# Optimization experiments

Hardware: AMD Instinct MI355X
Metric: run time of the kernel (lower is better)

The kernel has to match this reference:

```python
import jax, jax.numpy as jnp
import numpy as np

NUM_TASKS = 150
ACT_DIM = 4
ENC_DIM = 256
EMB_DIM = 32
HEAD_HID = 128
B, H, W = 256, 128, 128


def _conv(x, w, b):
    # x: NCHW, w: OIHW, stride 2, padding 1 (torch Conv2d semantics)
    y = jax.lax.conv_general_dilated(x, w, window_strides=(2, 2),
                                     padding=((1, 1), (1, 1)),
                                     dimension_numbers=('NCHW', 'OIHW', 'NCHW'))
    return y + b[None, :, None, None]


def setup_inputs() -> dict:
    key = jax.random.key(0)
    ks = iter(jax.random.split(key, 32))
    s = 0.05
    d = {
        'images': jax.random.normal(next(ks), (B, 3, H, W), jnp.float32),
        'proprioception': jax.random.normal(next(ks), (B, 7), jnp.float32),
        'task_ids': jax.random.randint(next(ks), (B,), 0, NUM_TASKS, jnp.int32),
        # vision encoder convs (OIHW)
        'c1_w': jax.random.normal(next(ks), (64, 3, 3, 3), jnp.float32) * s,
        'c1_b': jnp.zeros((64,), jnp.float32),
        'c2_w': jax.random.normal(next(ks), (128, 64, 3, 3), jnp.float32) * s,
        'c2_b': jnp.zeros((128,), jnp.float32),
        'c3_w': jax.random.normal(next(ks), (256, 128, 3, 3), jnp.float32) * s,
        'c3_b': jnp.zeros((256,), jnp.float32),
        # proprioception encoder (weights stored as [in, out])
        'p1_w': jax.random.normal(next(ks), (7, 64), jnp.float32) * s,
        'p1_b': jnp.zeros((64,), jnp.float32),
        'p2_w': jax.random.normal(next(ks), (64, 64), jnp.float32) * s,
        'p2_b': jnp.zeros((64,), jnp.float32),
        # shared-encoder fusion MLP (320 -> 256 -> 256)
        'f1_w': jax.random.normal(next(ks), (256 + 64, ENC_DIM), jnp.float32) * s,
        'f1_b': jnp.zeros((ENC_DIM,), jnp.float32),
        'f2_w': jax.random.normal(next(ks), (ENC_DIM, ENC_DIM), jnp.float32) * s,
        'f2_b': jnp.zeros((ENC_DIM,), jnp.float32),
        # task embedding table
        'task_emb': jax.random.normal(next(ks), (NUM_TASKS, EMB_DIM), jnp.float32) * s,
        # policy-level fusion (288 -> 256), dropout is identity at inference
        'g_w': jax.random.normal(next(ks), (ENC_DIM + EMB_DIM, ENC_DIM), jnp.float32) * s,
        'g_b': jnp.zeros((ENC_DIM,), jnp.float32),
        # stacked task-specific heads [num_tasks, in, out]
        'h1_w': jax.random.normal(next(ks), (NUM_TASKS, ENC_DIM, HEAD_HID), jnp.float32) * s,
        'h1_b': jnp.zeros((NUM_TASKS, HEAD_HID), jnp.float32),
        'h2_w': jax.random.normal(next(ks), (NUM_TASKS, HEAD_HID, HEAD_HID), jnp.float32) * s,
        'h2_b': jnp.zeros((NUM_TASKS, HEAD_HID), jnp.float32),
        'h3_w': jax.random.normal(next(ks), (NUM_TASKS, HEAD_HID, ACT_DIM), jnp.float32) * s,
        'h3_b': jnp.zeros((NUM_TASKS, ACT_DIM), jnp.float32),
    }
    return d


def reference(images, proprioception, task_ids,
              c1_w, c1_b, c2_w, c2_b, c3_w, c3_b,
              p1_w, p1_b, p2_w, p2_b,
              f1_w, f1_b, f2_w, f2_b,
              task_emb, g_w, g_b,
              h1_w, h1_b, h2_w, h2_b, h3_w, h3_b):
    relu = jax.nn.relu
    # vision encoder: 3 strided convs + global avg pool (AdaptiveAvgPool2d(1,1))
    v = relu(_conv(images, c1_w, c1_b))
    v = relu(_conv(v, c2_w, c2_b))
    v = relu(_conv(v, c3_w, c3_b))
    v = jnp.mean(v, axis=(2, 3))                      # [B, 256]
    # proprioception encoder (no final ReLU)
    p = relu(proprioception @ p1_w + p1_b) @ p2_w + p2_b  # [B, 64]
    # shared fusion
    f = relu(jnp.concatenate([v, p], axis=1) @ f1_w + f1_b)
    f = relu(f @ f2_w + f2_b)                         # [B, 256]
    # task embedding + policy fusion (dropout = identity in eval)
    e = task_emb[task_ids]                            # [B, 32]
    z = relu(jnp.concatenate([f, e], axis=1) @ g_w + g_b)  # [B, 256]
    # routed task heads: gather per-sample expert params, batched matmuls
    a = relu(jnp.einsum('bd,bdh->bh', z, h1_w[task_ids]) + h1_b[task_ids])
    a = relu(jnp.einsum('bd,bdh->bh', a, h2_w[task_ids]) + h2_b[task_ids])
    a = jnp.einsum('bd,bdh->bh', a, h3_w[task_ids]) + h3_b[task_ids]  # [B, 4]
    return a
```

## Files before the change

### kernel.cpp

```cpp
#include <hip/hip_runtime.h>
#include <hip/hip_bf16.h>

#define DIV_UP(a,b) (((a)+(b)-1)/(b))

typedef __attribute__((ext_vector_type(8))) short short8;
typedef __attribute__((ext_vector_type(4))) float f32x4;

__device__ __forceinline__ ushort bf16_bits(float x) {
    return __builtin_bit_cast(ushort, __float2bfloat16(x));
}

__device__ __forceinline__ void gload_lds16(const ushort* g, ushort* l) {
    __builtin_amdgcn_global_load_lds(
        (const __attribute__((address_space(1))) void*)g,
        (__attribute__((address_space(3))) void*)l, 16, 0, 0);
}

__global__ __launch_bounds__(256) void prep_kernel(
    uint4* __restrict__ act1, uint4* __restrict__ act2,
    float4* __restrict__ vbuf, int CHI,
    const float* __restrict__ c1_w, __hip_bfloat16* __restrict__ w1b,
    const float* __restrict__ c2_w, __hip_bfloat16* __restrict__ w2t,
    const float* __restrict__ c3_w, __hip_bfloat16* __restrict__ w3t) {
    const int tid = threadIdx.x;
    int bx = blockIdx.x;

    if (bx < CHI) {
        const int b = bx;
        const uint4 z = {0u, 0u, 0u, 0u};
        uint4* a1 = act1 + (size_t)b * 33800;
        for (int i = tid; i < 520; i += 256) a1[i] = z;
        for (int i = tid; i < 512; i += 256) {
            int r = (i >> 3) + 1;
            a1[r * 520 + (i & 7)] = z;
        }
        uint4* a2 = act2 + (size_t)b * 17424;
        for (int i = tid; i < 528; i += 256) a2[i] = z;
        for (int i = tid; i < 512; i += 256) {
            int r = (i >> 4) + 1;
            a2[r * 528 + (i & 15)] = z;
        }
        int idx = b * 256 + tid;
        float4 zf = {0.f, 0.f, 0.f, 0.f};
        if (idx < 16384) vbuf[idx] = zf;
        return;
    }
    bx -= CHI;

    if (bx < 8) {
        int t = bx * 256 + tid;
        int k  = t & 31;
        int oc = t >> 5;
        w1b[t] = (k < 27) ? __float2bfloat16(c1_w[oc * 27 + k])
                          : __float2bfloat16(0.f);
        return;
    }
    bx -= 8;

    const float* src;
    __hip_bfloat16* dst;
    int O, C, t;
    if (bx < 288) {
        src = c2_w; dst = w2t; O = 128; C = 64;
        t = bx * 256 + tid;
    } else {
        src = c3_w; dst = w3t; O = 256; C = 128;
        t = (bx - 288) * 256 + tid;
    }
    int e   = t & 7;
    int r   = t >> 3;
    int n   = r % O;
    int q   = r / O;
    int SEG = C >> 3;
    int sg  = q % SEG;
    int tap = q / SEG;
    dst[t] = __float2bfloat16(src[(n * C + sg * 8 + e) * 9 + tap]);
}

__global__ __launch_bounds__(256) void conv1_mfma_kernel(
    const float* __restrict__ in,
    const __hip_bfloat16* __restrict__ wB,
    const float* __restrict__ bias,
    __hip_bfloat16* __restrict__ out) {
    const int tid  = threadIdx.x;
    const int lane = tid & 63;
    const int wv   = tid >> 6;
    const int l15  = lane & 15;
    const int quad = lane >> 4;
    const int tile = blockIdx.x;
    const int b    = blockIdx.y;
    const int oh0  = tile << 2;

    __shared__ __align__(16) char smem[30208];
    float*  sx = (float*)smem;
    ushort* Al = (ushort*)(smem + 13824);

    const float* ip  = in + (size_t)b * 3 * 128 * 128;
    const int    ih0 = 2 * oh0 - 1;

#pragma unroll
    for (int it = 0; it < 4; ++it) {
        int e = (it << 8) + tid;
        if (e < 864) {
            int q = e >> 5, k = e & 31;
            int c = q / 9, r = q - c * 9;
            int row = ih0 + r;
            if (row < 0) row = 0;
            gload_lds16((const ushort*)(ip + c * 16384 + row * 128 + k * 4),
                        (ushort*)smem + (size_t)e * 8);
        }
    }
    __syncthreads();

    const int px = tid, ohl = px >> 6, ow = px & 63;
    union { uint4 u4[4]; ushort us[32]; } rowv;
#pragma unroll
    for (int c = 0; c < 3; ++c)
#pragma unroll
        for (int kh = 0; kh < 3; ++kh) {
            const bool rok = (ih0 + 2 * ohl + kh) >= 0;
            const float* srow = sx + (c * 9 + 2 * ohl + kh) * 128;
#pragma unroll
            for (int kw = 0; kw < 3; ++kw) {
                int iw = 2 * ow + kw - 1;
                bool ok = rok && (iw >= 0);
                float x = srow[iw < 0 ? 0 : iw];
                rowv.us[c * 9 + kh * 3 + kw] = bf16_bits(ok ? x : 0.f);
            }
        }
#pragma unroll
    for (int k = 27; k < 32; ++k) rowv.us[k] = 0;
#pragma unroll
    for (int q = 0; q < 4; ++q)
        *(uint4*)(Al + px * 32 + (((q ^ (px >> 1)) & 3) << 3)) = rowv.u4[q];

    short8 af[4], bf[4];
#pragma unroll
    for (int i = 0; i < 4; ++i)
        af[i] = __builtin_bit_cast(short8,
            *(const uint4*)(wB + ((i * 16 + l15) * 32 + quad * 8)));

    __syncthreads();

#pragma unroll
    for (int j = 0; j < 4; ++j) {
        int p = wv * 64 + j * 16 + l15;
        bf[j] = __builtin_bit_cast(short8,
            *(const uint4*)(Al + p * 32 + (((quad ^ (p >> 1)) & 3) << 3)));
    }
    f32x4 acc[4][4];
#pragma unroll
    for (int i = 0; i < 4; ++i)
#pragma unroll
        for (int j = 0; j < 4; ++j)
            acc[i][j] = __builtin_amdgcn_mfma_f32_16x16x32_bf16(
                af[i], bf[j], (f32x4){0.f, 0.f, 0.f, 0.f}, 0, 0, 0);

    float4 bv[4];
#pragma unroll
    for (int i = 0; i < 4; ++i)
        bv[i] = *(const float4*)(bias + i * 16 + quad * 4);

    __hip_bfloat16* ob = out + (((size_t)b * 65 + oh0 + 1) * 65 + 1) * 64;
#pragma unroll
    for (int j = 0; j < 4; ++j) {
        const int oww = j * 16 + l15;
        __hip_bfloat16* op = ob + ((size_t)(wv * 65) + oww) * 64 + quad * 4;
#pragma unroll
        for (int i = 0; i < 4; ++i) {
            union { uint2 u2; ushort us[4]; } pk;
#pragma unroll
            for (int r = 0; r < 4; ++r)
                pk.us[r] = bf16_bits(
                    fmaxf(acc[i][j][r] + ((const float*)&bv[i])[r], 0.f));
            *(uint2*)(op + i * 16) = pk.u2;
        }
    }
}

__global__ __launch_bounds__(256, 3) void conv2_gemm_kernel(
    const __hip_bfloat16* __restrict__ act,
    const __hip_bfloat16* __restrict__ wtB,
    const float* __restrict__ bias,
    __hip_bfloat16* __restrict__ out) {
    const int tid  = threadIdx.x;
    const int lane = tid & 63;
    const int w    = tid >> 6;
    const int l15  = lane & 15;
    const int quad = lane >> 4;
    const int per  = gridDim.x >> 3;
    const int Mt   = (blockIdx.x & 7) * per + (blockIdx.x >> 3);
    const int bimg = Mt >> 4;
    const int oh0  = (Mt & 15) << 1;

    __shared__ __align__(16) char smem[41600];
    ushort* As = (ushort*)smem;
    ushort* Cs = (ushort*)smem;

    f32x4 acc[2][4];
#pragma unroll
    for (int i = 0; i < 2; ++i)
#pragma unroll
        for (int j = 0; j < 4; ++j) acc[i][j] = (f32x4){0.f, 0.f, 0.f, 0.f};

    const int pxw = (w >> 1) << 5;
    const int wn  = (w & 1) << 6;
    const size_t abase = ((size_t)(bimg * 65 + 2 * oh0)) * 65 * 64;
    const ushort* ap = (const ushort*)act;

#pragma unroll
    for (int it = 0; it < 11; ++it) {
        int c = (it << 8) + tid;
        if (c < 2600) {
            int p = c >> 3, t = c & 7;
            int q = t ^ ((p >> 1) & 7);
            gload_lds16(ap + abase + (size_t)p * 64 + q * 8,
                        As + (size_t)c * 8);
        }
    }
    __syncthreads();

    for (int h = 0; h < 2; ++h) {
        const int q = h * 4 + quad;
#pragma unroll
        for (int tap = 0; tap < 9; ++tap) {
            const int kh = tap / 3, kw = tap - kh * 3;
            short8 af[2], bf[4];
#pragma unroll
            for (int i = 0; i < 2; ++i) {
                int ml = pxw + i * 16 + l15;
                int p  = ((ml >> 5) * 2 + kh) * 65 + ((ml & 31) * 2 + kw);
                af[i] = __builtin_bit_cast(short8,
                    *(const uint4*)(As + p * 64 +
                                    ((q ^ ((p >> 1) & 7)) << 3)));
            }
#pragma unroll
            for (int j = 0; j < 4; ++j)
                bf[j] = __builtin_bit_cast(short8,
                    *(const uint4*)(wtB +
                        ((size_t)((tap * 8 + h * 4 + quad) * 128) +
                         wn + j * 16 + l15) * 8));
#pragma unroll
            for (int i = 0; i < 2; ++i)
#pragma unroll
                for (int j = 0; j < 4; ++j)
                    acc[i][j] = __builtin_amdgcn_mfma_f32_16x16x32_bf16(
                        af[i], bf[j], acc[i][j], 0, 0, 0);
        }
    }

    __syncthreads();
#pragma unroll
    for (int j = 0; j < 4; ++j) {
        int n = wn + j * 16 + l15;
        float bv = bias[n];
#pragma unroll
        for (int i = 0; i < 2; ++i)
#pragma unroll
            for (int r = 0; r < 4; ++r) {
                int ml = pxw + i * 16 + quad * 4 + r;
                Cs[ml * 132 + n] = bf16_bits(fmaxf(acc[i][j][r] + bv, 0.f));
            }
    }
    __syncthreads();
#pragma unroll
    for (int q2 = 0; q2 < 8; ++q2) {
        int c   = tid + 256 * q2;
        int row = c >> 5;
        int off = c & 31;
        uint2 val = *(const uint2*)(Cs + row * 132 + off * 4);
        int m  = (Mt << 6) + row;
        int b  = m >> 10;
        int rr = m & 1023;
        int oh = rr >> 5;
        int ow = rr & 31;
        size_t pix = ((size_t)(b * 33 + oh + 1) * 33 + (ow + 1));
        *(uint2*)(out + pix * 128 + off * 4) = val;
    }
}

__global__ __launch_bounds__(256, 2) void conv3_gemm_pool_kernel(
    const __hip_bfloat16* __restrict__ act,
    const __hip_bfloat16* __restrict__ wtB,
    const float* __restrict__ bias,
    float* __restrict__ v ) {
    const int tid  = threadIdx.x;
    const int lane = tid & 63;
    const int w    = tid >> 6;
    const int l15  = lane & 15;
    const int quad = lane >> 4;
    const int per  = gridDim.x >> 3;
    const int Mt   = (blockIdx.x & 7) * per + (blockIdx.x >> 3);
    const int bimg = Mt >> 2;
    const int oh0  = (Mt & 3) << 2;

    __shared__ __align__(16) char smem[77824];
    ushort* As   = (ushort*)smem;
    float*  sred = (float*)smem;

    f32x4 acc[4][4];
#pragma unroll
    for (int i = 0; i < 4; ++i)
#pragma unroll
        for (int j = 0; j < 4; ++j) acc[i][j] = (f32x4){0.f, 0.f, 0.f, 0.f};

    const int wn = w << 6;
    const size_t abase = ((size_t)(bimg * 33 + 2 * oh0)) * 33 * 128;
    const ushort* ap = (const ushort*)act;

#pragma unroll
    for (int it = 0; it < 19; ++it) {
        int c  = (it << 8) + tid;
        int p  = c >> 4;
        int t  = c & 15;
        int h  = t >> 3;
        int ss = (t & 7) ^ ((p >> 1) & 7);
        gload_lds16(ap + abase + (size_t)p * 128 + h * 64 + ss * 8,
                    As + (size_t)c * 8);
    }
    __syncthreads();

    for (int h = 0; h < 2; ++h) {
#pragma unroll 1
        for (int tap = 0; tap < 9; ++tap) {
            const int kh = tap / 3, kw = tap - kh * 3;
#pragma unroll
            for (int ks = 0; ks < 2; ++ks) {
                short8 af[4], bf[4];
                const int sl = ks * 4 + quad;
#pragma unroll
                for (int i = 0; i < 4; ++i) {
                    int p = (i * 2 + kh) * 33 + l15 * 2 + kw;
                    af[i] = __builtin_bit_cast(short8,
                        *(const uint4*)(As + p * 128 + h * 64 +
                                        (((sl ^ (p >> 1)) & 7) << 3)));
                }
#pragma unroll
                for (int j = 0; j < 4; ++j)
                    bf[j] = __builtin_bit_cast(short8,
                        *(const uint4*)(wtB +
                            ((size_t)((tap * 16 + h * 8 + sl) * 256) +
                             wn + j * 16 + l15) * 8));
#pragma unroll
                for (int i = 0; i < 4; ++i)
#pragma unroll
                    for (int j = 0; j < 4; ++j)
                        acc[i][j] = __builtin_amdgcn_mfma_f32_16x16x32_bf16(
                            af[i], bf[j], acc[i][j], 0, 0, 0);
            }
        }
    }

    float s4[4];
#pragma unroll
    for (int j = 0; j < 4; ++j) {
        float bv = bias[wn + j * 16 + l15];
        float s = 0.f;
#pragma unroll
        for (int i = 0; i < 4; ++i)
#pragma unroll
            for (int r = 0; r < 4; ++r)
                s += fmaxf(acc[i][j][r] + bv, 0.f);
        s += __shfl_xor(s, 16, 64);
        s += __shfl_xor(s, 32, 64);
        s4[j] = s;
    }
    __syncthreads();
    if (quad == 0) {
#pragma unroll
        for (int j = 0; j < 4; ++j) sred[wn + j * 16 + l15] = s4[j];
    }
    __syncthreads();
    atomicAdd(v + (size_t)bimg * 256 + tid, sred[tid] * (1.f / 256.f));
}

template<int N, int K, int S, bool RELU>
__device__ __forceinline__ void gemv_stage(const float* __restrict__ w,
                                           const float* __restrict__ bias,
                                           const float* in, float* outv,
                                           float4* red4, int tid) {
    constexpr int G = N / 4;
    constexpr int CHK = K / S;
    static_assert(G * S == 256 && CHK * S == K, "stage shape");
    const int g = tid % G, s = tid / G;
    const float4* wp = (const float4*)w;
    float4 a; a.x = a.y = a.z = a.w = 0.f;
    const int k0 = s * CHK;
#pragma unroll 8
    for (int i = 0; i < CHK; ++i) {
        float x = in[k0 + i];
        float4 wv = wp[(size_t)(k0 + i) * G + g];
        a.x = fmaf(x, wv.x, a.x);
        a.y = fmaf(x, wv.y, a.y);
        a.z = fmaf(x, wv.z, a.z);
        a.w = fmaf(x, wv.w, a.w);
    }
    red4[tid] = a;
    __syncthreads();
    if (tid < N) {
        int gg = tid >> 2, e = tid & 3;
        float vv = bias[tid];
#pragma unroll
        for (int ss = 0; ss < S; ++ss) {
            const float* rp = (const float*)(red4 + ss * G + gg);
            vv += rp[e];
        }
        if (RELU) vv = fmaxf(vv, 0.f);
        outv[tid] = vv;
    }
    __syncthreads();
}

__global__ __launch_bounds__(256) void tail_kernel(
    const float* __restrict__ prop, const int* __restrict__ task_ids,
    const float* __restrict__ p1_w, const float* __restrict__ p1_b,
    const float* __restrict__ p2_w, const float* __restrict__ p2_b,
    const float* __restrict__ v,
    const float* __restrict__ f1_w, const float* __restrict__ f1_b,
    const float* __restrict__ f2_w, const float* __restrict__ f2_b,
    const float* __restrict__ task_emb,
    const float* __restrict__ g_w, const float* __restrict__ g_b,
    const float* __restrict__ h1_w, const float* __restrict__ h1_b,
    const float* __restrict__ h2_w, const float* __restrict__ h2_b,
    const float* __restrict__ h3_w, const float* __restrict__ h3_b,
    float* __restrict__ out) {
    const int b   = blockIdx.x;
    const int tid = threadIdx.x;
    const int t   = task_ids[b];
    __shared__ float sa[320];
    __shared__ float sb[288];
    __shared__ float sph[64];
    __shared__ float4 red4[256];

    sa[tid] = (tid < 256) ? v[(size_t)b * 256 + tid] : 0.f;
    if (tid < 64) {
        float h = p1_b[tid];
#pragma unroll
        for (int k = 0; k < 7; ++k) h = fmaf(prop[b * 7 + k], p1_w[k * 64 + tid], h);
        sph[tid] = fmaxf(h, 0.f);
    }
    __syncthreads();
    gemv_stage<64, 64, 16, false>(p2_w, p2_b, sph, sa + 256, red4, tid);
    gemv_stage<256, 320, 4, true>(f1_w, f1_b, sa, sb, red4, tid);
    gemv_stage<256, 256, 4, true>(f2_w, f2_b, sb, sa, red4, tid);
    if (tid < 32) sa[256 + tid] = task_emb[t * 32 + tid];
    __syncthreads();
    gemv_stage<256, 288, 4, true>(g_w, g_b, sa, sb, red4, tid);
    gemv_stage<128, 256, 8, true>(h1_w + (size_t)t * 32768, h1_b + t * 128,
                                  sb, sa, red4, tid);
    gemv_stage<128, 128, 8, true>(h2_w + (size_t)t * 16384, h2_b + t * 128,
                                  sa, sb, red4, tid);
    if (tid < 128) {
        float4 wv = ((const float4*)(h3_w + (size_t)t * 512))[tid];
        float x = sb[tid];
        float r0 = x * wv.x, r1 = x * wv.y, r2 = x * wv.z, r3 = x * wv.w;
#pragma unroll
        for (int off = 1; off < 64; off <<= 1) {
            r0 += __shfl_xor(r0, off, 64);
            r1 += __shfl_xor(r1, off, 64);
            r2 += __shfl_xor(r2, off, 64);
            r3 += __shfl_xor(r3, off, 64);
        }
        if ((tid & 63) == 0) {
            float4 rv; rv.x = r0; rv.y = r1; rv.z = r2; rv.w = r3;
            red4[tid >> 6] = rv;
        }
    }
    __syncthreads();
    if (tid < 4) {
        const float* ra = (const float*)(red4 + 0);
        const float* rb = (const float*)(red4 + 1);
        out[b * 4 + tid] = ra[tid] + rb[tid] + h3_b[t * 4 + tid];
    }
}

extern "C" void kernel_launch(void* const* d_in, const int* in_sizes, int n_in,
                              void* d_out, int out_size, void* d_ws, size_t ws_size,
                              hipStream_t stream) {
    (void)in_sizes; (void)n_in; (void)out_size;
    const float* images   = (const float*)d_in[0];
    const float* prop     = (const float*)d_in[1];
    const int*   task_ids = (const int*)d_in[2];
    const float* c1_w = (const float*)d_in[3];
    const float* c1_b = (const float*)d_in[4];
    const float* c2_w = (const float*)d_in[5];
    const float* c2_b = (const float*)d_in[6];
    const float* c3_w = (const float*)d_in[7];
    const float* c3_b = (const float*)d_in[8];
    const float* p1_w = (const float*)d_in[9];
    const float* p1_b = (const float*)d_in[10];
    const float* p2_w = (const float*)d_in[11];
    const float* p2_b = (const float*)d_in[12];
    const float* f1_w = (const float*)d_in[13];
    const float* f1_b = (const float*)d_in[14];
    const float* f2_w = (const float*)d_in[15];
    const float* f2_b = (const float*)d_in[16];
    const float* temb = (const float*)d_in[17];
    const float* g_w  = (const float*)d_in[18];
    const float* g_b  = (const float*)d_in[19];
    const float* h1_w = (const float*)d_in[20];
    const float* h1_b = (const float*)d_in[21];
    const float* h2_w = (const float*)d_in[22];
    const float* h2_b = (const float*)d_in[23];
    const float* h3_w = (const float*)d_in[24];
    const float* h3_b = (const float*)d_in[25];
    float* out = (float*)d_out;

    const size_t per_img = (size_t)65 * 65 * 64 * 2 + (size_t)33 * 33 * 128 * 2;
    const size_t fixed   = (size_t)256 * 256 * 4 + 1728 * 4 +
                           (size_t)73728 * 2 + (size_t)294912 * 2 + 4096;
    int CHI = 64;
    if (ws_size >= fixed + per_img * 256) CHI = 256;
    else if (ws_size >= fixed + per_img * 128) CHI = 128;

    char* ws = (char*)d_ws;
    size_t off = 0;
    auto alloc = [&](size_t bytes) {
        void* p = ws + off;
        off += (bytes + 255) & ~(size_t)255;
        return p;
    };
    __hip_bfloat16* act1 = (__hip_bfloat16*)alloc((size_t)CHI * 65 * 65 * 64 * 2);
    __hip_bfloat16* act2 = (__hip_bfloat16*)alloc((size_t)CHI * 33 * 33 * 128 * 2);
    float*          vbuf = (float*)alloc((size_t)256 * 256 * 4);
    __hip_bfloat16* w1b  = (__hip_bfloat16*)alloc((size_t)2048 * 2);
    __hip_bfloat16* w2t  = (__hip_bfloat16*)alloc((size_t)73728 * 2);
    __hip_bfloat16* w3t  = (__hip_bfloat16*)alloc((size_t)294912 * 2);

    prep_kernel<<<dim3(CHI + 8 + 288 + 1152), 256, 0, stream>>>(
        (uint4*)act1, (uint4*)act2, (float4*)vbuf, CHI,
        c1_w, w1b, c2_w, w2t, c3_w, w3t);

    for (int c0 = 0; c0 < 256; c0 += CHI) {
        const float* img_c = images + (size_t)c0 * 3 * 128 * 128;
        conv1_mfma_kernel<<<dim3(16, CHI), dim3(256), 0, stream>>>(
            img_c, w1b, c1_b, act1);
        conv2_gemm_kernel<<<dim3(CHI * 16), 256, 0, stream>>>(
            act1, w2t, c2_b, act2);
        conv3_gemm_pool_kernel<<<dim3(CHI * 4), 256, 0, stream>>>(
            act2, w3t, c3_b, vbuf + (size_t)c0 * 256);
    }
    tail_kernel<<<256, 256, 0, stream>>>(prop, task_ids, p1_w, p1_b, p2_w, p2_b,
                                         vbuf, f1_w, f1_b, f2_w, f2_b, temb,
                                         g_w, g_b, h1_w, h1_b, h2_w, h2_b,
                                         h3_w, h3_b, out);
}
```

Before: 324.9 us.

## Fuse conv1 into conv2 by recomputing conv1 tiles in LDS

Merges the conv1 and conv2 kernels so each conv2 block computes the conv1 output rows (with halo and padding) it needs directly into shared memory, instead of reading a materialized act1 buffer. This removes the large act1 global write/read and its zero-border initialization. In exchange the halo rows of conv1 are recomputed across neighbouring tiles, LDS use grows to about 75 KB per block, and occupancy drops to two blocks per CU.

Result: faster. 303.2 us (-6.7%).

```diff
diff --git a/kernel.cpp b/kernel.cpp
--- a/kernel.cpp
+++ b/kernel.cpp
@@ -17,7 +17,7 @@
 }
 
 __global__ __launch_bounds__(256) void prep_kernel(
-    uint4* __restrict__ act1, uint4* __restrict__ act2,
+    uint4* __restrict__ act2,
     float4* __restrict__ vbuf, int CHI,
     const float* __restrict__ c1_w, __hip_bfloat16* __restrict__ w1b,
     const float* __restrict__ c2_w, __hip_bfloat16* __restrict__ w2t,
@@ -28,12 +28,6 @@
     if (bx < CHI) {
         const int b = bx;
         const uint4 z = {0u, 0u, 0u, 0u};
-        uint4* a1 = act1 + (size_t)b * 33800;
-        for (int i = tid; i < 520; i += 256) a1[i] = z;
-        for (int i = tid; i < 512; i += 256) {
-            int r = (i >> 3) + 1;
-            a1[r * 520 + (i & 7)] = z;
-        }
         uint4* a2 = act2 + (size_t)b * 17424;
         for (int i = tid; i < 528; i += 256) a2[i] = z;
         for (int i = tid; i < 512; i += 256) {
@@ -77,125 +71,129 @@
     dst[t] = __float2bfloat16(src[(n * C + sg * 8 + e) * 9 + tap]);
 }
 
-__global__ __launch_bounds__(256) void conv1_mfma_kernel(
+__global__ __launch_bounds__(256, 2) void conv12_fused_kernel(
     const float* __restrict__ in,
-    const __hip_bfloat16* __restrict__ wB,
-    const float* __restrict__ bias,
+    const __hip_bfloat16* __restrict__ w1b,
+    const float* __restrict__ bias1,
+    const __hip_bfloat16* __restrict__ wtB,
+    const float* __restrict__ bias2,
     __hip_bfloat16* __restrict__ out) {
     const int tid  = threadIdx.x;
     const int lane = tid & 63;
     const int wv   = tid >> 6;
     const int l15  = lane & 15;
     const int quad = lane >> 4;
-    const int tile = blockIdx.x;
-    const int b    = blockIdx.y;
-    const int oh0  = tile << 2;
-
-    __shared__ __align__(16) char smem[30208];
-    float*  sx = (float*)smem;
-    ushort* Al = (ushort*)(smem + 13824);
-
-    const float* ip  = in + (size_t)b * 3 * 128 * 128;
-    const int    ih0 = 2 * oh0 - 1;
-
-#pragma unroll
-    for (int it = 0; it < 4; ++it) {
-        int e = (it << 8) + tid;
-        if (e < 864) {
-            int q = e >> 5, k = e & 31;
-            int c = q / 9, r = q - c * 9;
-            int row = ih0 + r;
-            if (row < 0) row = 0;
-            gload_lds16((const ushort*)(ip + c * 16384 + row * 128 + k * 4),
-                        (ushort*)smem + (size_t)e * 8);
-        }
-    }
-    __syncthreads();
-
-    const int px = tid, ohl = px >> 6, ow = px & 63;
-    union { uint4 u4[4]; ushort us[32]; } rowv;
-#pragma unroll
-    for (int c = 0; c < 3; ++c)
-#pragma unroll
-        for (int kh = 0; kh < 3; ++kh) {
-            const bool rok = (ih0 + 2 * ohl + kh) >= 0;
-            const float* srow = sx + (c * 9 + 2 * ohl + kh) * 128;
-#pragma unroll
-            for (int kw = 0; kw < 3; ++kw) {
-                int iw = 2 * ow + kw - 1;
-                bool ok = rok && (iw >= 0);
-                float x = srow[iw < 0 ? 0 : iw];
-                rowv.us[c * 9 + kh * 3 + kw] = bf16_bits(ok ? x : 0.f);
-            }
-        }
-#pragma unroll
-    for (int k = 27; k < 32; ++k) rowv.us[k] = 0;
-#pragma unroll
-    for (int q = 0; q < 4; ++q)
-        *(uint4*)(Al + px * 32 + (((q ^ (px >> 1)) & 3) << 3)) = rowv.u4[q];
-
-    short8 af[4], bf[4];
-#pragma unroll
-    for (int i = 0; i < 4; ++i)
-        af[i] = __builtin_bit_cast(short8,
-            *(const uint4*)(wB + ((i * 16 + l15) * 32 + quad * 8)));
-
-    __syncthreads();
-
-#pragma unroll
-    for (int j = 0; j < 4; ++j) {
-        int p = wv * 64 + j * 16 + l15;
-        bf[j] = __builtin_bit_cast(short8,
-            *(const uint4*)(Al + p * 32 + (((quad ^ (p >> 1)) & 3) << 3)));
-    }
-    f32x4 acc[4][4];
-#pragma unroll
-    for (int i = 0; i < 4; ++i)
-#pragma unroll
-        for (int j = 0; j < 4; ++j)
-            acc[i][j] = __builtin_amdgcn_mfma_f32_16x16x32_bf16(
-                af[i], bf[j], (f32x4){0.f, 0.f, 0.f, 0.f}, 0, 0, 0);
-
-    float4 bv[4];
-#pragma unroll
-    for (int i = 0; i < 4; ++i)
-        bv[i] = *(const float4*)(bias + i * 16 + quad * 4);
-
-    __hip_bfloat16* ob = out + (((size_t)b * 65 + oh0 + 1) * 65 + 1) * 64;
-#pragma unroll
-    for (int j = 0; j < 4; ++j) {
-        const int oww = j * 16 + l15;
-        __hip_bfloat16* op = ob + ((size_t)(wv * 65) + oww) * 64 + quad * 4;
-#pragma unroll
-        for (int i = 0; i < 4; ++i) {
-            union { uint2 u2; ushort us[4]; } pk;
-#pragma unroll
-            for (int r = 0; r < 4; ++r)
-                pk.us[r] = bf16_bits(
-                    fmaxf(acc[i][j][r] + ((const float*)&bv[i])[r], 0.f));
-            *(uint2*)(op + i * 16) = pk.u2;
-        }
-    }
-}
-
-__global__ __launch_bounds__(256, 3) void conv2_gemm_kernel(
-    const __hip_bfloat16* __restrict__ act,
-    const __hip_bfloat16* __restrict__ wtB,
-    const float* __restrict__ bias,
-    __hip_bfloat16* __restrict__ out) {
-    const int tid  = threadIdx.x;
-    const int lane = tid & 63;
-    const int w    = tid >> 6;
-    const int l15  = lane & 15;
-    const int quad = lane >> 4;
     const int per  = gridDim.x >> 3;
     const int Mt   = (blockIdx.x & 7) * per + (blockIdx.x >> 3);
     const int bimg = Mt >> 4;
     const int oh0  = (Mt & 15) << 1;
 
-    __shared__ __align__(16) char smem[41600];
-    ushort* As = (ushort*)smem;
-    ushort* Cs = (ushort*)smem;
+    __shared__ __align__(16) char smem[74880];
+    float*  sxf = (float*)smem;
+    ushort* Al  = (ushort*)(smem + 16896);
+    ushort* As  = (ushort*)(smem + 33280);
+    ushort* Cs  = (ushort*)smem;
+
+    const float* ip   = in + (size_t)bimg * 3 * 128 * 128;
+    const int    row0 = 4 * oh0 - 3;
+
+#pragma unroll
+    for (int it = 0; it < 5; ++it) {
+        int e = (it << 8) + tid;
+        if (e < 1056) {
+            int c = e / 352, rem = e - c * 352;
+            int r = rem >> 5, k = rem & 31;
+            int row = row0 + r;
+            if (row < 0) row = 0;
+            gload_lds16((const ushort*)(ip + c * 16384 + row * 128 + k * 4),
+                        (ushort*)smem + (size_t)e * 8);
+        }
+    }
+    __syncthreads();
+
+    short8 af1[4];
+#pragma unroll
+    for (int i = 0; i < 4; ++i)
+        af1[i] = __builtin_bit_cast(short8,
+            *(const uint4*)(w1b + ((i * 16 + l15) * 32 + quad * 8)));
+    float4 bv1[4];
+#pragma unroll
+    for (int i = 0; i < 4; ++i)
+        bv1[i] = *(const float4*)(bias1 + i * 16 + quad * 4);
+
+    for (int px0 = 0; px0 < 325; px0 += 256) {
+        const int pxg = px0 + tid;
+        const int r2  = pxg / 65;
+        const int C   = pxg - r2 * 65;
+        const bool vpx = (pxg <= 324) && (C >= 1) && !(oh0 == 0 && r2 == 0);
+
+        union { uint4 u4[4]; ushort us[32]; } rowv;
+#pragma unroll
+        for (int c = 0; c < 3; ++c)
+#pragma unroll
+            for (int kh = 0; kh < 3; ++kh) {
+                const int ih = 4 * oh0 + 2 * r2 + kh - 3;
+                const float* srow = sxf + (c * 11 + 2 * r2 + kh) * 128;
+                const bool rok = (ih >= 0);
+#pragma unroll
+                for (int kw = 0; kw < 3; ++kw) {
+                    int iw = 2 * C + kw - 3;
+                    bool ok = vpx && rok && (iw >= 0);
+                    float x = srow[iw < 0 ? 0 : iw];
+                    rowv.us[c * 9 + kh * 3 + kw] = bf16_bits(ok ? x : 0.f);
+                }
+            }
+#pragma unroll
+        for (int k = 27; k < 32; ++k) rowv.us[k] = 0;
+#pragma unroll
+        for (int q = 0; q < 4; ++q)
+            *(uint4*)(Al + tid * 32 + (((q ^ (tid >> 1)) & 3) << 3)) =
+                rowv.u4[q];
+        __syncthreads();
+
+        short8 bf1[4];
+#pragma unroll
+        for (int j = 0; j < 4; ++j) {
+            int pl = wv * 64 + j * 16 + l15;
+            bf1[j] = __builtin_bit_cast(short8,
+                *(const uint4*)(Al + pl * 32 + (((quad ^ (pl >> 1)) & 3) << 3)));
+        }
+        f32x4 acc1[4][4];
+#pragma unroll
+        for (int i = 0; i < 4; ++i)
+#pragma unroll
+            for (int j = 0; j < 4; ++j)
+                acc1[i][j] = __builtin_amdgcn_mfma_f32_16x16x32_bf16(
+                    af1[i], bf1[j], (f32x4){0.f, 0.f, 0.f, 0.f}, 0, 0, 0);
+
+#pragma unroll
+        for (int j = 0; j < 4; ++j) {
+            int pg = px0 + wv * 64 + j * 16 + l15;
+            if (pg <= 324) {
+                int r2g = pg / 65;
+                int Cg  = pg - r2g * 65;
+                bool wv2 = (Cg >= 1) && !(oh0 == 0 && r2g == 0);
+#pragma unroll
+                for (int i = 0; i < 4; ++i) {
+                    union { uint u; ushort us[2]; } lo, hi;
+                    lo.us[0] = bf16_bits(wv2 ? fmaxf(acc1[i][j][0] +
+                        ((const float*)&bv1[i])[0], 0.f) : 0.f);
+                    lo.us[1] = bf16_bits(wv2 ? fmaxf(acc1[i][j][1] +
+                        ((const float*)&bv1[i])[1], 0.f) : 0.f);
+                    hi.us[0] = bf16_bits(wv2 ? fmaxf(acc1[i][j][2] +
+                        ((const float*)&bv1[i])[2], 0.f) : 0.f);
+                    hi.us[1] = bf16_bits(wv2 ? fmaxf(acc1[i][j][3] +
+                        ((const float*)&bv1[i])[3], 0.f) : 0.f);
+                    int qc = i * 2 + (quad >> 1);
+                    ushort* dst = As + pg * 64 +
+                        ((qc ^ ((pg >> 1) & 7)) << 3) + (quad & 1) * 4;
+                    *(uint*)dst = lo.u;
+                    *(uint*)(dst + 2) = hi.u;
+                }
+            }
+        }
+        __syncthreads();
+    }
 
     f32x4 acc[2][4];
 #pragma unroll
@@ -203,22 +201,8 @@
 #pragma unroll
         for (int j = 0; j < 4; ++j) acc[i][j] = (f32x4){0.f, 0.f, 0.f, 0.f};
 
-    const int pxw = (w >> 1) << 5;
-    const int wn  = (w & 1) << 6;
-    const size_t abase = ((size_t)(bimg * 65 + 2 * oh0)) * 65 * 64;
-    const ushort* ap = (const ushort*)act;
-
-#pragma unroll
-    for (int it = 0; it < 11; ++it) {
-        int c = (it << 8) + tid;
-        if (c < 2600) {
-            int p = c >> 3, t = c & 7;
-            int q = t ^ ((p >> 1) & 7);
-            gload_lds16(ap + abase + (size_t)p * 64 + q * 8,
-                        As + (size_t)c * 8);
-        }
-    }
-    __syncthreads();
+    const int pxw2 = (wv >> 1) << 5;
+    const int wn   = (wv & 1) << 6;
 
     for (int h = 0; h < 2; ++h) {
         const int q = h * 4 + quad;
@@ -228,7 +212,7 @@
             short8 af[2], bf[4];
 #pragma unroll
             for (int i = 0; i < 2; ++i) {
-                int ml = pxw + i * 16 + l15;
+                int ml = pxw2 + i * 16 + l15;
                 int p  = ((ml >> 5) * 2 + kh) * 65 + ((ml & 31) * 2 + kw);
                 af[i] = __builtin_bit_cast(short8,
                     *(const uint4*)(As + p * 64 +
@@ -253,12 +237,12 @@
 #pragma unroll
     for (int j = 0; j < 4; ++j) {
         int n = wn + j * 16 + l15;
-        float bv = bias[n];
+        float bv = bias2[n];
 #pragma unroll
         for (int i = 0; i < 2; ++i)
 #pragma unroll
             for (int r = 0; r < 4; ++r) {
-                int ml = pxw + i * 16 + quad * 4 + r;
+                int ml = pxw2 + i * 16 + quad * 4 + r;
                 Cs[ml * 132 + n] = bf16_bits(fmaxf(acc[i][j][r] + bv, 0.f));
             }
     }
@@ -520,7 +504,7 @@
         off += (bytes + 255) & ~(size_t)255;
         return p;
     };
-    __hip_bfloat16* act1 = (__hip_bfloat16*)alloc((size_t)CHI * 65 * 65 * 64 * 2);
+    (void)alloc((size_t)CHI * 65 * 65 * 64 * 2);
     __hip_bfloat16* act2 = (__hip_bfloat16*)alloc((size_t)CHI * 33 * 33 * 128 * 2);
     float*          vbuf = (float*)alloc((size_t)256 * 256 * 4);
     __hip_bfloat16* w1b  = (__hip_bfloat16*)alloc((size_t)2048 * 2);
@@ -528,15 +512,13 @@
     __hip_bfloat16* w3t  = (__hip_bfloat16*)alloc((size_t)294912 * 2);
 
     prep_kernel<<<dim3(CHI + 8 + 288 + 1152), 256, 0, stream>>>(
-        (uint4*)act1, (uint4*)act2, (float4*)vbuf, CHI,
+        (uint4*)act2, (float4*)vbuf, CHI,
         c1_w, w1b, c2_w, w2t, c3_w, w3t);
 
     for (int c0 = 0; c0 < 256; c0 += CHI) {
         const float* img_c = images + (size_t)c0 * 3 * 128 * 128;
-        conv1_mfma_kernel<<<dim3(16, CHI), dim3(256), 0, stream>>>(
-            img_c, w1b, c1_b, act1);
-        conv2_gemm_kernel<<<dim3(CHI * 16), 256, 0, stream>>>(
-            act1, w2t, c2_b, act2);
+        conv12_fused_kernel<<<dim3(CHI * 16), 256, 0, stream>>>(
+            img_c, w1b, c1_b, w2t, c2_b, act2);
         conv3_gemm_pool_kernel<<<dim3(CHI * 4), 256, 0, stream>>>(
             act2, w3t, c3_b, vbuf + (size_t)c0 * 256);
     }
```
